# Optimization experiments

Measured on AMD Instinct MI355X. Metric: run time of the kernel, lower is better.

The kernel has to match this reference:

```python
import jax, jax.numpy as jnp
import numpy as np

DIM = 512
HEADS = 8
DH = DIM // HEADS
SCALE = DH ** -0.5
LN_EPS = 1e-5


def setup_inputs() -> dict:
    key = jax.random.key(0)
    ks = jax.random.split(key, 6)
    b, n = 16, 1024
    x = jax.random.normal(ks[0], (b, n, DIM), dtype=jnp.float32)
    # to_qkv: Linear(dim, 3*dim, bias=False)
    Wqkv = jax.random.normal(ks[1], (DIM, 3 * DIM), dtype=jnp.float32) * (DIM ** -0.5)
    # LayerNorm(inner_dim) affine params
    ln_g = jnp.ones((DIM,), dtype=jnp.float32)
    ln_b = jnp.zeros((DIM,), dtype=jnp.float32)
    # to_out: Linear(inner_dim, dim) with bias
    Wo = jax.random.normal(ks[2], (DIM, DIM), dtype=jnp.float32) * (DIM ** -0.5)
    bo = jnp.zeros((DIM,), dtype=jnp.float32)
    return {"x": x, "Wqkv": Wqkv, "ln_g": ln_g, "ln_b": ln_b, "Wo": Wo, "bo": bo}


def reference(x, Wqkv, ln_g, ln_b, Wo, bo):
    b, n, d = x.shape
    h, dh = HEADS, DH
    qkv = x @ Wqkv                              # [b, n, 3d]
    q, k, v = jnp.split(qkv, 3, axis=-1)        # each [b, n, d]
    def to_heads(t):
        return t.reshape(b, n, h, dh).transpose(0, 2, 1, 3)  # [b, h, n, dh]
    q, k, v = to_heads(q), to_heads(k), to_heads(v)
    dots = jnp.einsum('bhid,bhjd->bhij', q, k) * SCALE       # [b, h, n, n]
    attn = jax.nn.relu(dots)                                 # ReLU instead of softmax
    out = jnp.einsum('bhij,bhjd->bhid', attn, v)             # [b, h, n, dh]
    out = out.transpose(0, 2, 1, 3).reshape(b, n, d)         # [b, n, d]
    # LayerNorm over last dim
    mu = jnp.mean(out, axis=-1, keepdims=True)
    var = jnp.var(out, axis=-1, keepdims=True)
    out = (out - mu) * jax.lax.rsqrt(var + LN_EPS) * ln_g + ln_b
    return out @ Wo + bo
```

## Files before the change

kernel.cpp:

```cpp
#include <hip/hip_runtime.h>
#include <cstdint>
#include <cstddef>

typedef unsigned short u16;
typedef float f32x4 __attribute__((ext_vector_type(4)));
typedef short short8 __attribute__((ext_vector_type(8)));
typedef u16 u16x4 __attribute__((ext_vector_type(4)));

#define MFMA_BF16(acc, a, b) \
  asm("v_mfma_f32_16x16x32_bf16 %0, %1, %2, %0" : "+v"(acc) : "v"(a), "v"(b))

#define GLDS16(gp, lp) __builtin_amdgcn_global_load_lds( \
    (__attribute__((address_space(1))) void*)(void*)(uintptr_t)(gp), \
    (__attribute__((address_space(3))) void*)(lp), 16, 0, 0)

static __device__ __forceinline__ u16 f2bf(float f) {
  union { float f; unsigned u; } x; x.f = f;
  unsigned u = x.u + 0x7fffu + ((x.u >> 16) & 1u);
  return (u16)(u >> 16);
}

__global__ __launch_bounds__(256) void cvt_kernel(const float* __restrict__ src,
                                                  u16* __restrict__ dst, int n4) {
  int stride = gridDim.x * 256;
  for (int i = blockIdx.x * 256 + threadIdx.x; i < n4; i += stride) {
    f32x4 v = ((const f32x4*)src)[i];
    u16x4 o;
    o[0] = f2bf(v[0]); o[1] = f2bf(v[1]); o[2] = f2bf(v[2]); o[3] = f2bf(v[3]);
    ((u16x4*)dst)[i] = o;
  }
}

__global__ __launch_bounds__(256) void tcvt_kernel(const float* __restrict__ src,
                                                   u16* __restrict__ dst, int R, int C,
                                                   int sclim) {
  __shared__ float tile[64][65];
  int c0 = blockIdx.x * 64, r0 = blockIdx.y * 64;
  for (int t = threadIdx.x; t < 4096; t += 256) {
    int r = t >> 6, c = t & 63;
    tile[r][c] = src[(size_t)(r0 + r) * C + c0 + c];
  }
  __syncthreads();
  for (int t = threadIdx.x; t < 4096; t += 256) {
    int rr = t >> 6, cc = t & 63;
    float sc = (c0 + rr) < sclim ? 0.125f : 1.0f;
    dst[(size_t)(c0 + rr) * R + r0 + cc] = f2bf(tile[cc][rr] * sc);
  }
}

__global__ __launch_bounds__(256) void gemm_qkv_kernel(const u16* __restrict__ A,
                                                       const u16* __restrict__ BT,
                                                       u16* __restrict__ qk,
                                                       u16* __restrict__ vT) {
  __shared__ u16 smem[16896];
  u16* As = smem;
  u16* Bs = smem + 8192;
  const int tid = threadIdx.x, lane = tid & 63, wave = tid >> 6;
  const int wr = wave >> 1, wc = wave & 1;
  const int bid = blockIdx.x;
  const int lin = (bid & 7) * 192 + (bid >> 3);
  const int my = lin / 12, nx = lin - my * 12;
  const int m0 = my * 128, n0 = nx * 128;
  f32x4 acc[4][4] = {};
  for (int kt = 0; kt < 8; ++kt) {
    int k0 = kt * 64;
    __syncthreads();
    #pragma unroll
    for (int t = 0; t < 4; ++t) {
      int ch = wave * 4 + t;
      GLDS16(A + (size_t)(m0 + ch * 8 + (lane >> 3)) * 512 + k0 + (lane & 7) * 8, &As[ch * 512]);
      GLDS16(BT + (size_t)(n0 + ch * 8 + (lane >> 3)) * 512 + k0 + (lane & 7) * 8, &Bs[ch * 512]);
    }
    __syncthreads();
    #pragma unroll
    for (int kk = 0; kk < 2; ++kk) {
      short8 af[4], bfr[4];
      #pragma unroll
      for (int m = 0; m < 4; ++m)
        af[m] = *(const short8*)&As[(wr * 64 + m * 16 + (lane & 15)) * 64 + kk * 32 + (lane >> 4) * 8];
      #pragma unroll
      for (int n = 0; n < 4; ++n)
        bfr[n] = *(const short8*)&Bs[(wc * 64 + n * 16 + (lane & 15)) * 64 + kk * 32 + (lane >> 4) * 8];
      #pragma unroll
      for (int m = 0; m < 4; ++m)
        #pragma unroll
        for (int n = 0; n < 4; ++n)
          MFMA_BF16(acc[m][n], af[m], bfr[n]);
    }
  }
  const int row0 = m0 + wr * 64, col0 = n0 + wc * 64;
  if (n0 < 1024) {
    #pragma unroll
    for (int m = 0; m < 4; ++m) {
      int row = row0 + m * 16 + (lane >> 4) * 4;
      #pragma unroll
      for (int n = 0; n < 4; ++n) {
        int col = col0 + n * 16 + (lane & 15);
        #pragma unroll
        for (int i = 0; i < 4; ++i)
          qk[(size_t)(row + i) * 1024 + col] = f2bf(acc[m][n][i]);
      }
    }
  } else {
    __syncthreads();
    const int lo = lane & 15, g = lane >> 4;
    #pragma unroll
    for (int m = 0; m < 4; ++m) {
      int tl0 = wr * 64 + m * 16 + g * 4;
      #pragma unroll
      for (int n = 0; n < 4; ++n) {
        int dl = wc * 64 + n * 16 + lo;
        u16x4 pk;
        #pragma unroll
        for (int i = 0; i < 4; ++i) pk[i] = f2bf(acc[m][n][i]);
        *(u16x4*)&smem[dl * 132 + tl0] = pk;
      }
    }
    __syncthreads();
    const int bb = m0 >> 10, nn0 = m0 & 1023, d0 = n0 - 1024;
    for (int t = tid; t < 128 * 32; t += 256) {
      int d = t >> 5, sg = t & 31;
      u16x4 v = *(const u16x4*)&smem[d * 132 + sg * 4];
      *(u16x4*)&vT[(size_t)(bb * 512 + d0 + d) * 1024 + nn0 + sg * 4] = v;
    }
  }
}

__global__ __launch_bounds__(256) void attn_kernel(const u16* __restrict__ qk,
                                                   const u16* __restrict__ vT,
                                                   float* __restrict__ aout) {
  __shared__ u16 smem[24576];
  u16* Ks = smem;
  u16* Ss = smem;
  u16* Vs = smem + 16384;
  const int tid = threadIdx.x, lane = tid & 63, wave = tid >> 6;
  const int wr = wave >> 1, wc = wave & 1;
  const int L = blockIdx.x;
  const int qt = L >> 7, bh = L & 127, h = bh & 7, b = bh >> 3;
  const size_t qrow0 = (size_t)b * 1024 + qt * 128;

  short8 qf[4][2];
  #pragma unroll
  for (int m = 0; m < 4; ++m)
    #pragma unroll
    for (int kk = 0; kk < 2; ++kk)
      qf[m][kk] = *(const short8*)&qk[(qrow0 + wr * 64 + m * 16 + (lane & 15)) * 1024
                                      + h * 64 + kk * 32 + (lane >> 4) * 8];
  f32x4 acc[4][2] = {};
  for (int jt = 0; jt < 8; ++jt) {
    __syncthreads();
    const u16* Kg = qk + ((size_t)b * 1024 + jt * 128) * 1024 + 512 + h * 64;
    const u16* Vg = vT + ((size_t)b * 512 + h * 64) * 1024 + jt * 128;
    #pragma unroll
    for (int t = 0; t < 4; ++t) {
      int ch = wave * 4 + t;
      GLDS16(Kg + (size_t)(ch * 8 + (lane >> 3)) * 1024 + ((lane & 7) ^ (lane >> 3)) * 8,
             &Ks[ch * 512]);
      GLDS16(Vg + (size_t)(ch * 4 + (lane >> 4)) * 1024 + ((lane & 15) ^ (t * 4 + (lane >> 4))) * 8,
             &Vs[ch * 512]);
    }
    __syncthreads();
    f32x4 sacc[4][4] = {};
    __builtin_amdgcn_s_setprio(1);
    #pragma unroll
    for (int kk = 0; kk < 2; ++kk) {
      short8 kf[4];
      #pragma unroll
      for (int n = 0; n < 4; ++n) {
        int r = wc * 64 + n * 16 + (lane & 15);
        int slot = kk * 4 + (lane >> 4);
        kf[n] = *(const short8*)&Ks[r * 64 + ((slot ^ (r & 7)) * 8)];
      }
      #pragma unroll
      for (int n = 0; n < 4; ++n)
        #pragma unroll
        for (int m = 0; m < 4; ++m)
          MFMA_BF16(sacc[n][m], kf[n], qf[m][kk]);
    }
    __builtin_amdgcn_s_setprio(0);
    __syncthreads();
    #pragma unroll
    for (int m = 0; m < 4; ++m) {
      int i = wr * 64 + m * 16 + (lane & 15);
      unsigned rowbase = (unsigned)i * 256;
      unsigned sw = (unsigned)(i & 15) << 4;
      #pragma unroll
      for (int n = 0; n < 4; ++n) {
        int j0 = wc * 64 + n * 16 + (lane >> 4) * 4;
        u16x4 pk;
        #pragma unroll
        for (int r = 0; r < 4; ++r) pk[r] = f2bf(fmaxf(sacc[n][m][r], 0.f));
        *(u16x4*)((char*)Ss + (rowbase + (((unsigned)j0 * 2) ^ sw))) = pk;
      }
    }
    __syncthreads();
    __builtin_amdgcn_s_setprio(1);
    #pragma unroll
    for (int ks = 0; ks < 4; ++ks) {
      short8 sa[4], vb[2];
      #pragma unroll
      for (int m = 0; m < 4; ++m) {
        int i = wr * 64 + m * 16 + (lane & 15);
        unsigned c2 = (unsigned)(ks * 32 + (lane >> 4) * 8) * 2;
        sa[m] = *(const short8*)((const char*)Ss + (unsigned)i * 256 + (c2 ^ ((unsigned)(i & 15) << 4)));
      }
      #pragma unroll
      for (int n = 0; n < 2; ++n) {
        int r = wc * 32 + n * 16 + (lane & 15);
        int slot = ks * 4 + (lane >> 4);
        vb[n] = *(const short8*)&Vs[r * 128 + ((slot ^ (r & 15)) * 8)];
      }
      #pragma unroll
      for (int m = 0; m < 4; ++m)
        #pragma unroll
        for (int n = 0; n < 2; ++n)
          MFMA_BF16(acc[m][n], sa[m], vb[n]);
    }
    __builtin_amdgcn_s_setprio(0);
  }
  #pragma unroll
  for (int m = 0; m < 4; ++m) {
    int row = wr * 64 + m * 16 + (lane >> 4) * 4;
    #pragma unroll
    for (int n = 0; n < 2; ++n) {
      int col = h * 64 + wc * 32 + n * 16 + (lane & 15);
      #pragma unroll
      for (int i = 0; i < 4; ++i)
        aout[(qrow0 + row + i) * 512 + col] = acc[m][n][i];
    }
  }
}

__global__ __launch_bounds__(256) void ln_kernel(const float* __restrict__ x,
                                                 const float* __restrict__ g,
                                                 const float* __restrict__ bt,
                                                 u16* __restrict__ y) {
  const int lane = threadIdx.x & 63, wave = threadIdx.x >> 6;
  const size_t row = (size_t)blockIdx.x * 4 + wave;
  const float* xr = x + row * 512;
  f32x4 v0 = *(const f32x4*)&xr[lane * 4];
  f32x4 v1 = *(const f32x4*)&xr[256 + lane * 4];
  float s = v0[0] + v0[1] + v0[2] + v0[3] + v1[0] + v1[1] + v1[2] + v1[3];
  float q = v0[0]*v0[0] + v0[1]*v0[1] + v0[2]*v0[2] + v0[3]*v0[3]
          + v1[0]*v1[0] + v1[1]*v1[1] + v1[2]*v1[2] + v1[3]*v1[3];
  #pragma unroll
  for (int o = 32; o > 0; o >>= 1) { s += __shfl_xor(s, o); q += __shfl_xor(q, o); }
  float mean = s * (1.f / 512.f);
  float var  = q * (1.f / 512.f) - mean * mean;
  float rstd = rsqrtf(var + 1e-5f);
  f32x4 g0 = *(const f32x4*)&g[lane * 4],  g1 = *(const f32x4*)&g[256 + lane * 4];
  f32x4 b0 = *(const f32x4*)&bt[lane * 4], b1 = *(const f32x4*)&bt[256 + lane * 4];
  u16x4 o0, o1;
  #pragma unroll
  for (int i = 0; i < 4; ++i) {
    o0[i] = f2bf((v0[i] - mean) * rstd * g0[i] + b0[i]);
    o1[i] = f2bf((v1[i] - mean) * rstd * g1[i] + b1[i]);
  }
  *(u16x4*)&y[row * 512 + lane * 4] = o0;
  *(u16x4*)&y[row * 512 + 256 + lane * 4] = o1;
}

__global__ __launch_bounds__(256) void gemm_out_kernel(const u16* __restrict__ A,
                                                       const u16* __restrict__ BT,
                                                       const float* __restrict__ bias,
                                                       float* __restrict__ out) {
  __shared__ u16 As[128 * 64];
  __shared__ u16 Bs[128 * 64];
  const int tid = threadIdx.x, lane = tid & 63, wave = tid >> 6;
  const int wr = wave >> 1, wc = wave & 1;
  const int bid = blockIdx.x;
  const int lin = (bid & 7) * 64 + (bid >> 3);
  const int m0 = (lin >> 2) * 128, n0 = (lin & 3) * 128;
  f32x4 acc[4][4] = {};
  for (int kt = 0; kt < 8; ++kt) {
    int k0 = kt * 64;
    __syncthreads();
    #pragma unroll
    for (int t = 0; t < 4; ++t) {
      int ch = wave * 4 + t;
      GLDS16(A + (size_t)(m0 + ch * 8 + (lane >> 3)) * 512 + k0 + (lane & 7) * 8, &As[ch * 512]);
      GLDS16(BT + (size_t)(n0 + ch * 8 + (lane >> 3)) * 512 + k0 + (lane & 7) * 8, &Bs[ch * 512]);
    }
    __syncthreads();
    #pragma unroll
    for (int kk = 0; kk < 2; ++kk) {
      short8 af[4], bfr[4];
      #pragma unroll
      for (int m = 0; m < 4; ++m)
        af[m] = *(const short8*)&As[(wr * 64 + m * 16 + (lane & 15)) * 64 + kk * 32 + (lane >> 4) * 8];
      #pragma unroll
      for (int n = 0; n < 4; ++n)
        bfr[n] = *(const short8*)&Bs[(wc * 64 + n * 16 + (lane & 15)) * 64 + kk * 32 + (lane >> 4) * 8];
      #pragma unroll
      for (int m = 0; m < 4; ++m)
        #pragma unroll
        for (int n = 0; n < 4; ++n)
          MFMA_BF16(acc[m][n], af[m], bfr[n]);
    }
  }
  const int row0 = m0 + wr * 64, col0 = n0 + wc * 64;
  #pragma unroll
  for (int m = 0; m < 4; ++m) {
    int row = row0 + m * 16 + (lane >> 4) * 4;
    #pragma unroll
    for (int n = 0; n < 4; ++n) {
      int col = col0 + n * 16 + (lane & 15);
      float bv = bias[col];
      #pragma unroll
      for (int i = 0; i < 4; ++i)
        out[(size_t)(row + i) * 512 + col] = acc[m][n][i] + bv;
    }
  }
}

extern "C" void kernel_launch(void* const* d_in, const int* in_sizes, int n_in,
                              void* d_out, int out_size, void* d_ws, size_t ws_size,
                              hipStream_t stream) {
  const float* x    = (const float*)d_in[0];
  const float* Wqkv = (const float*)d_in[1];
  const float* ln_g = (const float*)d_in[2];
  const float* ln_b = (const float*)d_in[3];
  const float* Wo   = (const float*)d_in[4];
  const float* bo   = (const float*)d_in[5];
  float* out = (float*)d_out;
  char* ws = (char*)d_ws;

  u16*   xbf   = (u16*)(ws);
  u16*   wqkvt = (u16*)(ws + 16777216);
  u16*   wot   = (u16*)(ws + 18350080);
  u16*   qkb   = (u16*)(ws + 18874368);
  u16*   vtb   = (u16*)(ws + 52428800);
  float* att   = (float*)(ws + 69206016);

  cvt_kernel<<<4096, 256, 0, stream>>>(x, xbf, 8388608 / 4);
  tcvt_kernel<<<dim3(24, 8), 256, 0, stream>>>(Wqkv, wqkvt, 512, 1536, 512);
  tcvt_kernel<<<dim3(8, 8), 256, 0, stream>>>(Wo, wot, 512, 512, 0);
  gemm_qkv_kernel<<<1536, 256, 0, stream>>>(xbf, wqkvt, qkb, vtb);
  attn_kernel<<<1024, 256, 0, stream>>>(qkb, vtb, att);
  ln_kernel<<<4096, 256, 0, stream>>>(att, ln_g, ln_b, xbf);
  gemm_out_kernel<<<512, 256, 0, stream>>>(xbf, wot, bo, out);
}
```

Baseline: 130.8 us.

## Shrink attention LDS, preload V fragments to registers, store bf16 attention output

The attention kernel's shared buffer is cut from 24576 to 16384 elements by placing V right after K and reusing the K region for the score tile. This works because V fragments and the ReLU'd bf16 scores are now loaded into registers before the barrier that precedes the score writes. Launch bounds now request 4 blocks per SM for higher occupancy, at the cost of more register pressure from the held fragments. The attention output is written as bf16 instead of fp32, halving LayerNorm input traffic but adding rounding before normalization.

```diff
diff --git a/kernel.cpp b/kernel.cpp
--- a/kernel.cpp
+++ b/kernel.cpp
@@ -126,13 +126,13 @@
   }
 }
 
-__global__ __launch_bounds__(256) void attn_kernel(const u16* __restrict__ qk,
-                                                   const u16* __restrict__ vT,
-                                                   float* __restrict__ aout) {
-  __shared__ u16 smem[24576];
+__global__ __launch_bounds__(256, 4) void attn_kernel(const u16* __restrict__ qk,
+                                                      const u16* __restrict__ vT,
+                                                      u16* __restrict__ aout) {
+  __shared__ u16 smem[16384];
   u16* Ks = smem;
+  u16* Vs = smem + 8192;
   u16* Ss = smem;
-  u16* Vs = smem + 16384;
   const int tid = threadIdx.x, lane = tid & 63, wave = tid >> 6;
   const int wr = wave >> 1, wc = wave & 1;
   const int L = blockIdx.x;
@@ -178,6 +178,23 @@
           MFMA_BF16(sacc[n][m], kf[n], qf[m][kk]);
     }
     __builtin_amdgcn_s_setprio(0);
+    u16x4 pk[4][4];
+    #pragma unroll
+    for (int n = 0; n < 4; ++n)
+      #pragma unroll
+      for (int m = 0; m < 4; ++m)
+        #pragma unroll
+        for (int r = 0; r < 4; ++r)
+          pk[n][m][r] = f2bf(fmaxf(sacc[n][m][r], 0.f));
+    short8 vbr[4][2];
+    #pragma unroll
+    for (int ks = 0; ks < 4; ++ks)
+      #pragma unroll
+      for (int n = 0; n < 2; ++n) {
+        int r = wc * 32 + n * 16 + (lane & 15);
+        int slot = ks * 4 + (lane >> 4);
+        vbr[ks][n] = *(const short8*)&Vs[r * 128 + ((slot ^ (r & 15)) * 8)];
+      }
     __syncthreads();
     #pragma unroll
     for (int m = 0; m < 4; ++m) {
@@ -187,17 +204,14 @@
       #pragma unroll
       for (int n = 0; n < 4; ++n) {
         int j0 = wc * 64 + n * 16 + (lane >> 4) * 4;
-        u16x4 pk;
-        #pragma unroll
-        for (int r = 0; r < 4; ++r) pk[r] = f2bf(fmaxf(sacc[n][m][r], 0.f));
-        *(u16x4*)((char*)Ss + (rowbase + (((unsigned)j0 * 2) ^ sw))) = pk;
+        *(u16x4*)((char*)Ss + (rowbase + (((unsigned)j0 * 2) ^ sw))) = pk[n][m];
       }
     }
     __syncthreads();
     __builtin_amdgcn_s_setprio(1);
     #pragma unroll
     for (int ks = 0; ks < 4; ++ks) {
-      short8 sa[4], vb[2];
+      short8 sa[4];
       #pragma unroll
       for (int m = 0; m < 4; ++m) {
         int i = wr * 64 + m * 16 + (lane & 15);
@@ -205,16 +219,10 @@
         sa[m] = *(const short8*)((const char*)Ss + (unsigned)i * 256 + (c2 ^ ((unsigned)(i & 15) << 4)));
       }
       #pragma unroll
-      for (int n = 0; n < 2; ++n) {
-        int r = wc * 32 + n * 16 + (lane & 15);
-        int slot = ks * 4 + (lane >> 4);
-        vb[n] = *(const short8*)&Vs[r * 128 + ((slot ^ (r & 15)) * 8)];
-      }
-      #pragma unroll
       for (int m = 0; m < 4; ++m)
         #pragma unroll
         for (int n = 0; n < 2; ++n)
-          MFMA_BF16(acc[m][n], sa[m], vb[n]);
+          MFMA_BF16(acc[m][n], sa[m], vbr[ks][n]);
     }
     __builtin_amdgcn_s_setprio(0);
   }
@@ -226,38 +234,45 @@
       int col = h * 64 + wc * 32 + n * 16 + (lane & 15);
       #pragma unroll
       for (int i = 0; i < 4; ++i)
-        aout[(qrow0 + row + i) * 512 + col] = acc[m][n][i];
-    }
-  }
-}
-
-__global__ __launch_bounds__(256) void ln_kernel(const float* __restrict__ x,
+        aout[(qrow0 + row + i) * 512 + col] = f2bf(acc[m][n][i]);
+    }
+  }
+}
+
+__global__ __launch_bounds__(256) void ln_kernel(const u16* __restrict__ x,
                                                  const float* __restrict__ g,
                                                  const float* __restrict__ bt,
                                                  u16* __restrict__ y) {
   const int lane = threadIdx.x & 63, wave = threadIdx.x >> 6;
   const size_t row = (size_t)blockIdx.x * 4 + wave;
-  const float* xr = x + row * 512;
-  f32x4 v0 = *(const f32x4*)&xr[lane * 4];
-  f32x4 v1 = *(const f32x4*)&xr[256 + lane * 4];
-  float s = v0[0] + v0[1] + v0[2] + v0[3] + v1[0] + v1[1] + v1[2] + v1[3];
-  float q = v0[0]*v0[0] + v0[1]*v0[1] + v0[2]*v0[2] + v0[3]*v0[3]
-          + v1[0]*v1[0] + v1[1]*v1[1] + v1[2]*v1[2] + v1[3]*v1[3];
+  const u16* xr = x + row * 512;
+  u16x4 h0 = *(const u16x4*)&xr[lane * 8];
+  u16x4 h1 = *(const u16x4*)&xr[lane * 8 + 4];
+  float v[8];
+  #pragma unroll
+  for (int i = 0; i < 4; ++i) {
+    union { unsigned u; float f; } a, bu;
+    a.u = (unsigned)h0[i] << 16;  v[i] = a.f;
+    bu.u = (unsigned)h1[i] << 16; v[4 + i] = bu.f;
+  }
+  float s = 0.f, q = 0.f;
+  #pragma unroll
+  for (int i = 0; i < 8; ++i) { s += v[i]; q += v[i] * v[i]; }
   #pragma unroll
   for (int o = 32; o > 0; o >>= 1) { s += __shfl_xor(s, o); q += __shfl_xor(q, o); }
   float mean = s * (1.f / 512.f);
   float var  = q * (1.f / 512.f) - mean * mean;
   float rstd = rsqrtf(var + 1e-5f);
-  f32x4 g0 = *(const f32x4*)&g[lane * 4],  g1 = *(const f32x4*)&g[256 + lane * 4];
-  f32x4 b0 = *(const f32x4*)&bt[lane * 4], b1 = *(const f32x4*)&bt[256 + lane * 4];
+  f32x4 g0 = *(const f32x4*)&g[lane * 8],  g1 = *(const f32x4*)&g[lane * 8 + 4];
+  f32x4 b0 = *(const f32x4*)&bt[lane * 8], b1 = *(const f32x4*)&bt[lane * 8 + 4];
   u16x4 o0, o1;
   #pragma unroll
   for (int i = 0; i < 4; ++i) {
-    o0[i] = f2bf((v0[i] - mean) * rstd * g0[i] + b0[i]);
-    o1[i] = f2bf((v1[i] - mean) * rstd * g1[i] + b1[i]);
-  }
-  *(u16x4*)&y[row * 512 + lane * 4] = o0;
-  *(u16x4*)&y[row * 512 + 256 + lane * 4] = o1;
+    o0[i] = f2bf((v[i] - mean) * rstd * g0[i] + b0[i]);
+    o1[i] = f2bf((v[4 + i] - mean) * rstd * g1[i] + b1[i]);
+  }
+  *(u16x4*)&y[row * 512 + lane * 8] = o0;
+  *(u16x4*)&y[row * 512 + lane * 8 + 4] = o1;
 }
 
 __global__ __launch_bounds__(256) void gemm_out_kernel(const u16* __restrict__ A,
@@ -330,7 +345,7 @@
   u16*   wot   = (u16*)(ws + 18350080);
   u16*   qkb   = (u16*)(ws + 18874368);
   u16*   vtb   = (u16*)(ws + 52428800);
-  float* att   = (float*)(ws + 69206016);
+  u16*   att   = (u16*)(ws + 69206016);
 
   cvt_kernel<<<4096, 256, 0, stream>>>(x, xbf, 8388608 / 4);
   tcvt_kernel<<<dim3(24, 8), 256, 0, stream>>>(Wqkv, wqkvt, 512, 1536, 512);
```

Result: slower. 194.8 us (+48.9%).
